# Optimization experiments

Measured on AMD Instinct MI355X. Metric: run time of the kernel, lower is better.

Reference implementation:

```python
import jax, jax.numpy as jnp
import numpy as np

L, K, H = 8192, 30, 128
SCALE = 30.0
LN_EPS = 1e-5


def _ln(x, g, b):
    mu = jnp.mean(x, axis=-1, keepdims=True)
    var = jnp.mean((x - mu) ** 2, axis=-1, keepdims=True)
    return (x - mu) * jax.lax.rsqrt(var + LN_EPS) * g + b


def _gelu(x):
    return jax.nn.gelu(x, approximate=False)  # torch.nn.GELU default (exact)


def setup_inputs() -> dict:
    key = jax.random.key(0)
    ks = jax.random.split(key, 16)

    def lin(k, din, dout):
        k1, k2 = jax.random.split(k)
        w = jax.random.normal(k1, (din, dout), jnp.float32) / np.sqrt(din).astype(np.float32)
        b = jax.random.normal(k2, (dout,), jnp.float32) * 0.01
        return w, b

    inp = {}
    inp['h_V'] = jax.random.normal(ks[0], (L, H), jnp.float32)
    inp['h_E'] = jax.random.normal(ks[1], (L, K, H), jnp.float32)
    inp['E_idx'] = jax.random.randint(ks[2], (L, K), 0, L, jnp.int32)
    inp['mask_V'] = jnp.ones((L,), jnp.float32)
    inp['mask_attend'] = jnp.ones((L, K), jnp.float32)

    D_in = 3 * H  # num_hidden + num_in = 128 + 256
    inp['W1'], inp['b1'] = lin(ks[3], D_in, H)
    inp['W2'], inp['b2'] = lin(ks[4], H, H)
    inp['W3'], inp['b3'] = lin(ks[5], H, H)
    inp['W11'], inp['b11'] = lin(ks[6], D_in, H)
    inp['W12'], inp['b12'] = lin(ks[7], H, H)
    inp['W13'], inp['b13'] = lin(ks[8], H, H)
    inp['Wi'], inp['bi'] = lin(ks[9], H, 4 * H)   # PositionWiseFeedForward.W_in
    inp['Wo'], inp['bo'] = lin(ks[10], 4 * H, H)  # PositionWiseFeedForward.W_out
    inp['g1'] = jnp.ones((H,), jnp.float32); inp['be1'] = jnp.zeros((H,), jnp.float32)
    inp['g2'] = jnp.ones((H,), jnp.float32); inp['be2'] = jnp.zeros((H,), jnp.float32)
    inp['g3'] = jnp.ones((H,), jnp.float32); inp['be3'] = jnp.zeros((H,), jnp.float32)
    return inp


def _forward(h_V, h_E, E_idx, mask_V, mask_attend,
             W1, b1, W2, b2, W3, b3, W11, b11, W12, b12, W13, b13,
             Wi, bi, Wo, bo, g1, be1, g2, be2, g3, be3):
    # --- node update: gather neighbors, concat, 3-layer MLP message, masked sum ---
    h_nb = h_V[E_idx]                                   # [L,K,H] gather_nodes
    h_EV = jnp.concatenate(
        [jnp.broadcast_to(h_V[:, None, :], (L, K, H)), h_E, h_nb], axis=-1)  # [L,K,3H]
    m = _gelu(h_EV @ W1 + b1)
    m = _gelu(m @ W2 + b2)
    m = m @ W3 + b3                                     # [L,K,H]
    m = mask_attend[..., None] * m
    dh = jnp.sum(m, axis=-2) / SCALE                    # [L,H]
    h_V = _ln(h_V + dh, g1, be1)
    # --- position-wise FFN ---
    dh = _gelu(h_V @ Wi + bi) @ Wo + bo
    h_V = _ln(h_V + dh, g2, be2)
    h_V = mask_V[:, None] * h_V
    # --- edge update ---
    h_nb = h_V[E_idx]
    h_EV = jnp.concatenate(
        [jnp.broadcast_to(h_V[:, None, :], (L, K, H)), h_E, h_nb], axis=-1)
    m = _gelu(h_EV @ W11 + b11)
    m = _gelu(m @ W12 + b12)
    m = m @ W13 + b13
    h_E = _ln(h_E + m, g3, be3)
    return h_V, h_E


def reference(h_V, h_E, E_idx, mask_V, mask_attend,
              W1, b1, W2, b2, W3, b3, W11, b11, W12, b12, W13, b13,
              Wi, bi, Wo, bo, g1, be1, g2, be2, g3, be3):
    return _forward(h_V, h_E, E_idx, mask_V, mask_attend,
                    W1, b1, W2, b2, W3, b3, W11, b11, W12, b12, W13, b13,
                    Wi, bi, Wo, bo, g1, be1, g2, be2, g3, be3)
```

## Files before the change

### kernel.cpp

```cpp
#include <hip/hip_runtime.h>
#include <math.h>

typedef unsigned short u16;
typedef __bf16 bf16x8 __attribute__((ext_vector_type(8)));
typedef float f32x4 __attribute__((ext_vector_type(4)));
typedef u16 u16x8 __attribute__((ext_vector_type(8)));

#define LTOT 8192
#define KNB  30
#define HDIM 128

__device__ __forceinline__ float bf2f(u16 u){
  unsigned x = ((unsigned)u) << 16;
  return __builtin_bit_cast(float, x);
}
__device__ __forceinline__ u16 f2bf(float f){
  __bf16 h = (__bf16)f;
  return __builtin_bit_cast(u16, h);
}
__device__ __forceinline__ float fast_exp2(float x){
#if __has_builtin(__builtin_amdgcn_exp2f)
  return __builtin_amdgcn_exp2f(x);
#else
  return exp2f(x);
#endif
}
__device__ __forceinline__ float gelu_f(float x){
  float x2 = x * x;
  float g  = x * (2.3022082f + 0.10294324f * x2);
  float e  = fast_exp2(g);
  float r  = __builtin_amdgcn_rcpf(e + 1.f);
  return x * (1.f - r);
}
__device__ __forceinline__ void pack8(u16* dst, const float* s){
  float4 a = *(const float4*)s, b = *(const float4*)(s + 4);
  u16x8 p;
  p[0]=f2bf(a.x); p[1]=f2bf(a.y); p[2]=f2bf(a.z); p[3]=f2bf(a.w);
  p[4]=f2bf(b.x); p[5]=f2bf(b.y); p[6]=f2bf(b.z); p[7]=f2bf(b.w);
  *(u16x8*)dst = p;
}

struct TEnt { const float* src; u16* dst; int K; int N; int nb; };
struct TTab { TEnt e[12]; };

__global__ __launch_bounds__(256) void transpose_kernel(TTab t){
  int b = (int)blockIdx.x;
  for (int i = 0; i < 12; ++i){
    int nb = t.e[i].nb;
    if (b < nb){
      int N = t.e[i].N, Kd = t.e[i].K;
      int idx = b * 256 + (int)threadIdx.x;
      if (idx < Kd * N){
        int k = idx / N;
        int n = idx - k * N;
        t.e[i].dst[n * Kd + k] = f2bf(t.e[i].src[(long)k * N + n]);
      }
      return;
    }
    b -= nb;
  }
}

template<bool XF32>
__global__ __launch_bounds__(256) void pre_gemm_kernel(
  const void* __restrict__ X,
  const u16* __restrict__ WTa, const float* __restrict__ ba, u16* __restrict__ outa,
  const u16* __restrict__ WTc, u16* __restrict__ outc)
{
  __shared__ __align__(16) char smem[8704];
  u16* Xs = (u16*)smem;
  const int tid = threadIdx.x;
  const int wave = tid >> 6, lane = tid & 63, q = lane >> 4, s = lane & 15;
  const int row0 = (int)blockIdx.x * 32;

  for (int i = tid; i < 32 * 16; i += 256){
    int r = i >> 4, cb = i & 15;
    if (XF32) pack8(&Xs[r * 136 + cb * 8], &((const float*)X)[(long)(row0 + r) * HDIM + cb * 8]);
    else *(u16x8*)&Xs[r * 136 + cb * 8] = *(const u16x8*)&((const u16*)X)[(long)(row0 + r) * HDIM + cb * 8];
  }
  __syncthreads();
  for (int w = 0; w < 2; ++w){
    const u16* W = w ? WTc : WTa;
    u16* out = w ? outc : outa;
    f32x4 acc[2][2];
#pragma unroll
    for (int mt = 0; mt < 2; ++mt)
#pragma unroll
      for (int nt = 0; nt < 2; ++nt){ f32x4 z = {0.f,0.f,0.f,0.f}; acc[mt][nt] = z; }
    for (int kt = 0; kt < 4; ++kt){
      bf16x8 b0 = *(const bf16x8*)&W[(wave * 32 + s) * 128 + kt * 32 + q * 8];
      bf16x8 b1 = *(const bf16x8*)&W[(wave * 32 + 16 + s) * 128 + kt * 32 + q * 8];
#pragma unroll
      for (int mt = 0; mt < 2; ++mt){
        bf16x8 af = *(const bf16x8*)&Xs[(mt * 16 + s) * 136 + kt * 32 + q * 8];
        acc[mt][0] = __builtin_amdgcn_mfma_f32_16x16x32_bf16(af, b0, acc[mt][0], 0, 0, 0);
        acc[mt][1] = __builtin_amdgcn_mfma_f32_16x16x32_bf16(af, b1, acc[mt][1], 0, 0, 0);
      }
    }
#pragma unroll
    for (int nt = 0; nt < 2; ++nt){
      int col = wave * 32 + nt * 16 + s;
      float bv = w ? 0.f : ba[col];
#pragma unroll
      for (int mt = 0; mt < 2; ++mt)
#pragma unroll
        for (int r = 0; r < 4; ++r){
          int row = row0 + mt * 16 + q * 4 + r;
          out[(long)row * HDIM + col] = f2bf(acc[mt][nt][r] + bv);
        }
    }
  }
}

template<bool EDGE>
__global__ __launch_bounds__(256, 4) void msg_kernel(
  const float* __restrict__ hVin,
  const float* __restrict__ hE,
  const int* __restrict__ Eidx,
  const float* __restrict__ maskA,
  const u16* __restrict__ vsum,
  const u16* __restrict__ vcg,
  const u16* __restrict__ WTb, const u16* __restrict__ WT2, const u16* __restrict__ WT3,
  const float* __restrict__ b2, const float* __restrict__ b3,
  const float* __restrict__ gam, const float* __restrict__ bet,
  float* __restrict__ out_f32,
  u16* __restrict__ out_b16,
  float* __restrict__ outE)
{
  __shared__ __align__(16) char smem[36352];
  u16*   As   = (u16*)smem;
  float* ovl  = (float*)smem;
  u16*   Vs   = (u16*)(smem + 17408);
  float* vbuf = (float*)(smem + 34816);
  float* mbuf = (float*)(smem + 35840);
  int*   nbr  = (int*)(smem + 36096);

  const int tid = threadIdx.x;
  const int wave = tid >> 6, lane = tid & 63, q = lane >> 4, s = lane & 15;
  const int node0 = (int)blockIdx.x * 2;

  for (int i = tid; i < 64 * 16; i += 256){
    int r = i >> 4, cb = i & 15, nd = r >> 5, k = r & 31;
    if (k < KNB)
      pack8(&As[r * 136 + cb * 8], &hE[(((long)(node0 + nd) * KNB) + k) * HDIM + cb * 8]);
    else { u16x8 z = {0,0,0,0,0,0,0,0}; *(u16x8*)&As[r * 136 + cb * 8] = z; }
  }
  if (tid < 64){
    int nd = tid >> 5, k = tid & 31;
    int e = (node0 + nd) * KNB + k;
    bool v = (k < KNB);
    nbr[tid] = v ? Eidx[e] : 0;
    if (!EDGE) mbuf[tid] = v ? maskA[e] : 0.f;
  }
  vbuf[tid] = bf2f(vsum[(long)(node0 + (tid >> 7)) * HDIM + (tid & 127)]);

  __syncthreads();

  for (int i = tid; i < 64 * 16; i += 256){
    int r = i >> 4, cb = i & 15;
    *(u16x8*)&Vs[r * 136 + cb * 8] = *(const u16x8*)&vcg[(long)nbr[r] * HDIM + cb * 8];
  }

  f32x4 acc[4][2];
  for (int layer = 0; layer < 3; ++layer){
    const u16* W = (layer == 0) ? WTb : ((layer == 1) ? WT2 : WT3);
    if (layer) __syncthreads();
#pragma unroll
    for (int mt = 0; mt < 4; ++mt){ f32x4 z = {0.f,0.f,0.f,0.f}; acc[mt][0] = z; acc[mt][1] = z; }
    for (int kt = 0; kt < 4; ++kt){
      bf16x8 b0 = *(const bf16x8*)&W[(wave * 32 + s) * 128 + kt * 32 + q * 8];
      bf16x8 b1 = *(const bf16x8*)&W[(wave * 32 + 16 + s) * 128 + kt * 32 + q * 8];
#pragma unroll
      for (int mt = 0; mt < 4; ++mt){
        bf16x8 af = *(const bf16x8*)&As[(mt * 16 + s) * 136 + kt * 32 + q * 8];
        acc[mt][0] = __builtin_amdgcn_mfma_f32_16x16x32_bf16(af, b0, acc[mt][0], 0, 0, 0);
        acc[mt][1] = __builtin_amdgcn_mfma_f32_16x16x32_bf16(af, b1, acc[mt][1], 0, 0, 0);
      }
    }
    if (layer < 2){
      __syncthreads();
#pragma unroll
      for (int nt = 0; nt < 2; ++nt){
        int col = wave * 32 + nt * 16 + s;
        float bv = (layer == 1) ? b2[col] : 0.f;
        float vb0 = 0.f, vb1 = 0.f;
        if (layer == 0){ vb0 = vbuf[col]; vb1 = vbuf[128 + col]; }
#pragma unroll
        for (int mt = 0; mt < 4; ++mt)
#pragma unroll
          for (int r = 0; r < 4; ++r){
            int row = mt * 16 + q * 4 + r;
            float v = acc[mt][nt][r] + bv;
            if (layer == 0)
              v += (mt < 2 ? vb0 : vb1) + bf2f(Vs[row * 136 + col]);
            As[row * 136 + col] = f2bf(gelu_f(v));
          }
      }
    }
  }
  __syncthreads();

  if (!EDGE){
    float* dh = ovl;
#pragma unroll
    for (int nt = 0; nt < 2; ++nt){
      int col = wave * 32 + nt * 16 + s;
      float b3v = b3[col];
#pragma unroll
      for (int ni = 0; ni < 2; ++ni){
        float ss = 0.f;
#pragma unroll
        for (int mh = 0; mh < 2; ++mh){
          int mt = ni * 2 + mh;
#pragma unroll
          for (int r = 0; r < 4; ++r){
            int row = mt * 16 + q * 4 + r;
            ss += (acc[mt][nt][r] + b3v) * mbuf[row];
          }
        }
        ss += __shfl_xor(ss, 16);
        ss += __shfl_xor(ss, 32);
        if (q == 0) dh[ni * 128 + col] = ss * (1.f / 30.f);
      }
    }
    __syncthreads();
    if (wave < 2){
      int node = node0 + wave;
      float x0 = hVin[(long)node * HDIM + lane]      + dh[wave * 128 + lane];
      float x1 = hVin[(long)node * HDIM + 64 + lane] + dh[wave * 128 + 64 + lane];
      float sm = x0 + x1, s2 = x0 * x0 + x1 * x1;
#pragma unroll
      for (int o = 32; o; o >>= 1){ sm += __shfl_xor(sm, o); s2 += __shfl_xor(s2, o); }
      float mu = sm * (1.f / 128.f);
      float var = fmaxf(s2 * (1.f / 128.f) - mu * mu, 0.f);
      float rs = rsqrtf(var + 1e-5f);
      float y0 = (x0 - mu) * rs * gam[lane]      + bet[lane];
      float y1 = (x1 - mu) * rs * gam[64 + lane] + bet[64 + lane];
      out_f32[(long)node * HDIM + lane]      = y0;
      out_f32[(long)node * HDIM + 64 + lane] = y1;
      out_b16[(long)node * HDIM + lane]      = f2bf(y0);
      out_b16[(long)node * HDIM + 64 + lane] = f2bf(y1);
    }
  } else {
    float* part  = ovl;
    float* part2 = ovl + 256;
    float* muv   = ovl + 512;
    float* rsv   = ovl + 576;
#pragma unroll
    for (int nt = 0; nt < 2; ++nt){
      int col = wave * 32 + nt * 16 + s;
      float b3v = b3[col];
#pragma unroll
      for (int mt = 0; mt < 4; ++mt)
#pragma unroll
        for (int r = 0; r < 4; ++r){
          int row = mt * 16 + q * 4 + r, nd = row >> 5, k = row & 31;
          float z = acc[mt][nt][r] + b3v;
          if (k < KNB) z += hE[(((long)(node0 + nd) * KNB) + k) * HDIM + col];
          acc[mt][nt][r] = z;
        }
    }
#pragma unroll
    for (int mt = 0; mt < 4; ++mt)
#pragma unroll
      for (int r = 0; r < 4; ++r){
        int row = mt * 16 + q * 4 + r;
        float ps = acc[mt][0][r] + acc[mt][1][r];
        float pq = acc[mt][0][r] * acc[mt][0][r] + acc[mt][1][r] * acc[mt][1][r];
#pragma unroll
        for (int o = 1; o < 16; o <<= 1){ ps += __shfl_xor(ps, o); pq += __shfl_xor(pq, o); }
        if (s == 0){ part[row * 4 + wave] = ps; part2[row * 4 + wave] = pq; }
      }
    __syncthreads();
    if (tid < 64){
      float sm = part[tid*4] + part[tid*4+1] + part[tid*4+2] + part[tid*4+3];
      float sq = part2[tid*4] + part2[tid*4+1] + part2[tid*4+2] + part2[tid*4+3];
      float mu = sm * (1.f / 128.f);
      float var = fmaxf(sq * (1.f / 128.f) - mu * mu, 0.f);
      muv[tid] = mu;
      rsv[tid] = rsqrtf(var + 1e-5f);
    }
    __syncthreads();
#pragma unroll
    for (int nt = 0; nt < 2; ++nt){
      int col = wave * 32 + nt * 16 + s;
      float gv = gam[col], bv = bet[col];
#pragma unroll
      for (int mt = 0; mt < 4; ++mt)
#pragma unroll
        for (int r = 0; r < 4; ++r){
          int row = mt * 16 + q * 4 + r, nd = row >> 5, k = row & 31;
          if (k < KNB){
            float y = (acc[mt][nt][r] - muv[row]) * rsv[row] * gv + bv;
            outE[(((long)(node0 + nd) * KNB) + k) * HDIM + col] = y;
          }
        }
    }
  }
}

__global__ __launch_bounds__(256) void ffn_kernel(
  const u16* __restrict__ xb, const float* __restrict__ xf,
  const u16* __restrict__ WiT,
  const u16* __restrict__ WoT,
  const float* __restrict__ bi, const float* __restrict__ bo,
  const float* __restrict__ g2, const float* __restrict__ be2,
  const float* __restrict__ maskV,
  float* __restrict__ outV, u16* __restrict__ hv2)
{
  __shared__ __align__(16) char smem[18816];
  u16*   Xs = (u16*)smem;
  u16*   Ts = (u16*)(smem + 8704);
  float* part  = (float*)(smem + 17408);
  float* part2 = part + 128;
  float* muv   = part + 256;
  float* rsv   = part + 288;
  const int tid = threadIdx.x;
  const int wave = tid >> 6, lane = tid & 63, q = lane >> 4, s = lane & 15;
  const int row0 = (int)blockIdx.x * 32;

  for (int i = tid; i < 32 * 16; i += 256){
    int r = i >> 4, cb = i & 15;
    *(u16x8*)&Xs[r * 136 + cb * 8] = *(const u16x8*)&xb[(long)(row0 + r) * HDIM + cb * 8];
  }
  f32x4 yac[2][2];
#pragma unroll
  for (int mt = 0; mt < 2; ++mt)
#pragma unroll
    for (int nt = 0; nt < 2; ++nt){ f32x4 z = {0.f,0.f,0.f,0.f}; yac[mt][nt] = z; }

  for (int j = 0; j < 4; ++j){
    __syncthreads();
    f32x4 tac[2][2];
#pragma unroll
    for (int mt = 0; mt < 2; ++mt)
#pragma unroll
      for (int nt = 0; nt < 2; ++nt){ f32x4 z = {0.f,0.f,0.f,0.f}; tac[mt][nt] = z; }
    for (int kt = 0; kt < 4; ++kt){
      bf16x8 b0 = *(const bf16x8*)&WiT[((long)(j * 128 + wave * 32 + s)) * 128 + kt * 32 + q * 8];
      bf16x8 b1 = *(const bf16x8*)&WiT[((long)(j * 128 + wave * 32 + 16 + s)) * 128 + kt * 32 + q * 8];
#pragma unroll
      for (int mt = 0; mt < 2; ++mt){
        bf16x8 af = *(const bf16x8*)&Xs[(mt * 16 + s) * 136 + kt * 32 + q * 8];
        tac[mt][0] = __builtin_amdgcn_mfma_f32_16x16x32_bf16(af, b0, tac[mt][0], 0, 0, 0);
        tac[mt][1] = __builtin_amdgcn_mfma_f32_16x16x32_bf16(af, b1, tac[mt][1], 0, 0, 0);
      }
    }
#pragma unroll
    for (int nt = 0; nt < 2; ++nt){
      int col = wave * 32 + nt * 16 + s;
      float bv = bi[j * 128 + col];
#pragma unroll
      for (int mt = 0; mt < 2; ++mt)
#pragma unroll
        for (int r = 0; r < 4; ++r){
          int row = mt * 16 + q * 4 + r;
          Ts[row * 136 + col] = f2bf(gelu_f(tac[mt][nt][r] + bv));
        }
    }
    __syncthreads();
    for (int kt = 0; kt < 4; ++kt){
      bf16x8 b0 = *(const bf16x8*)&WoT[((long)(wave * 32 + s)) * 512 + j * 128 + kt * 32 + q * 8];
      bf16x8 b1 = *(const bf16x8*)&WoT[((long)(wave * 32 + 16 + s)) * 512 + j * 128 + kt * 32 + q * 8];
#pragma unroll
      for (int mt = 0; mt < 2; ++mt){
        bf16x8 af = *(const bf16x8*)&Ts[(mt * 16 + s) * 136 + kt * 32 + q * 8];
        yac[mt][0] = __builtin_amdgcn_mfma_f32_16x16x32_bf16(af, b0, yac[mt][0], 0, 0, 0);
        yac[mt][1] = __builtin_amdgcn_mfma_f32_16x16x32_bf16(af, b1, yac[mt][1], 0, 0, 0);
      }
    }
  }
#pragma unroll
  for (int nt = 0; nt < 2; ++nt){
    int col = wave * 32 + nt * 16 + s;
    float bv = bo[col];
#pragma unroll
    for (int mt = 0; mt < 2; ++mt)
#pragma unroll
      for (int r = 0; r < 4; ++r){
        int row = mt * 16 + q * 4 + r;
        yac[mt][nt][r] += bv + xf[(long)(row0 + row) * HDIM + col];
      }
  }
#pragma unroll
  for (int mt = 0; mt < 2; ++mt)
#pragma unroll
    for (int r = 0; r < 4; ++r){
      int row = mt * 16 + q * 4 + r;
      float ps = yac[mt][0][r] + yac[mt][1][r];
      float pq = yac[mt][0][r] * yac[mt][0][r] + yac[mt][1][r] * yac[mt][1][r];
#pragma unroll
      for (int o = 1; o < 16; o <<= 1){ ps += __shfl_xor(ps, o); pq += __shfl_xor(pq, o); }
      if (s == 0){ part[row * 4 + wave] = ps; part2[row * 4 + wave] = pq; }
    }
  __syncthreads();
  if (tid < 32){
    float sm = part[tid*4] + part[tid*4+1] + part[tid*4+2] + part[tid*4+3];
    float sq = part2[tid*4] + part2[tid*4+1] + part2[tid*4+2] + part2[tid*4+3];
    float mu = sm * (1.f / 128.f);
    float var = fmaxf(sq * (1.f / 128.f) - mu * mu, 0.f);
    muv[tid] = mu;
    rsv[tid] = rsqrtf(var + 1e-5f);
  }
  __syncthreads();
#pragma unroll
  for (int nt = 0; nt < 2; ++nt){
    int col = wave * 32 + nt * 16 + s;
    float gv = g2[col], bv = be2[col];
#pragma unroll
    for (int mt = 0; mt < 2; ++mt)
#pragma unroll
      for (int r = 0; r < 4; ++r){
        int row = mt * 16 + q * 4 + r;
        float y = (yac[mt][nt][r] - muv[row]) * rsv[row] * gv + bv;
        y *= maskV[row0 + row];
        outV[(long)(row0 + row) * HDIM + col] = y;
        hv2[(long)(row0 + row) * HDIM + col] = f2bf(y);
      }
  }
}

extern "C" void kernel_launch(void* const* d_in, const int* in_sizes, int n_in,
                              void* d_out, int out_size, void* d_ws, size_t ws_size,
                              hipStream_t stream) {
  const float* hV    = (const float*)d_in[0];
  const float* hE    = (const float*)d_in[1];
  const int*   Eidx  = (const int*)d_in[2];
  const float* maskV = (const float*)d_in[3];
  const float* maskA = (const float*)d_in[4];
  const float* W1  = (const float*)d_in[5];  const float* b1  = (const float*)d_in[6];
  const float* W2  = (const float*)d_in[7];  const float* b2  = (const float*)d_in[8];
  const float* W3  = (const float*)d_in[9];  const float* b3  = (const float*)d_in[10];
  const float* W11 = (const float*)d_in[11]; const float* b11 = (const float*)d_in[12];
  const float* W12 = (const float*)d_in[13]; const float* b12 = (const float*)d_in[14];
  const float* W13 = (const float*)d_in[15]; const float* b13 = (const float*)d_in[16];
  const float* Wi  = (const float*)d_in[17]; const float* bi  = (const float*)d_in[18];
  const float* Wo  = (const float*)d_in[19]; const float* bo  = (const float*)d_in[20];
  const float* g1  = (const float*)d_in[21]; const float* be1 = (const float*)d_in[22];
  const float* g2  = (const float*)d_in[23]; const float* be2 = (const float*)d_in[24];
  const float* g3  = (const float*)d_in[25]; const float* be3 = (const float*)d_in[26];

  char* ws = (char*)d_ws;
  u16* wt = (u16*)ws;
  u16* wtW1a  = wt;
  u16* wtW1b  = wt + 16384;
  u16* wtW1c  = wt + 32768;
  u16* wtW2   = wt + 49152;
  u16* wtW3   = wt + 65536;
  u16* wtW11a = wt + 81920;
  u16* wtW11b = wt + 98304;
  u16* wtW11c = wt + 114688;
  u16* wtW12  = wt + 131072;
  u16* wtW13  = wt + 147456;
  u16* wtWi   = wt + 163840;
  u16* wtWo   = wt + 229376;
  size_t off = 589824;
  u16* vsum1   = (u16*)(ws + off); off += 2097152;
  u16* vc      = (u16*)(ws + off); off += 2097152;
  u16* vsum11  = (u16*)(ws + off); off += 2097152;
  u16* vc2     = (u16*)(ws + off); off += 2097152;
  float* hv1_f32 = (float*)(ws + off); off += 4194304;
  u16*   hv1_b16 = (u16*)(ws + off);   off += 2097152;
  u16*   hv2_b16 = (u16*)(ws + off);   off += 2097152;

  float* outV = (float*)d_out;
  float* outE = (float*)d_out + (long)LTOT * HDIM;

  TTab tt;
  tt.e[0]  = { W1,          wtW1a,  128, 128, 64 };
  tt.e[1]  = { W1 + 16384,  wtW1b,  128, 128, 64 };
  tt.e[2]  = { W1 + 32768,  wtW1c,  128, 128, 64 };
  tt.e[3]  = { W2,          wtW2,   128, 128, 64 };
  tt.e[4]  = { W3,          wtW3,   128, 128, 64 };
  tt.e[5]  = { W11,         wtW11a, 128, 128, 64 };
  tt.e[6]  = { W11 + 16384, wtW11b, 128, 128, 64 };
  tt.e[7]  = { W11 + 32768, wtW11c, 128, 128, 64 };
  tt.e[8]  = { W12,         wtW12,  128, 128, 64 };
  tt.e[9]  = { W13,         wtW13,  128, 128, 64 };
  tt.e[10] = { Wi,          wtWi,   128, 512, 256 };
  tt.e[11] = { Wo,          wtWo,   512, 128, 256 };
  transpose_kernel<<<dim3(1152), dim3(256), 0, stream>>>(tt);

  pre_gemm_kernel<true><<<dim3(256), dim3(256), 0, stream>>>(
      hV, wtW1a, b1, vsum1, wtW1c, vc);
  msg_kernel<false><<<dim3(4096), dim3(256), 0, stream>>>(
      hV, hE, Eidx, maskA, vsum1, vc, wtW1b, wtW2, wtW3, b2, b3, g1, be1,
      hv1_f32, hv1_b16, nullptr);
  ffn_kernel<<<dim3(256), dim3(256), 0, stream>>>(
      hv1_b16, hv1_f32, wtWi, wtWo, bi, bo, g2, be2, maskV, outV, hv2_b16);
  pre_gemm_kernel<false><<<dim3(256), dim3(256), 0, stream>>>(
      hv2_b16, wtW11a, b11, vsum11, wtW11c, vc2);
  msg_kernel<true><<<dim3(4096), dim3(256), 0, stream>>>(
      hV, hE, Eidx, maskA, vsum11, vc2, wtW11b, wtW12, wtW13, b12, b13, g3, be3,
      hv1_f32, hv1_b16, outE);
}
```

Before: 442.5 us.

## Fuse second pre-GEMM into FFN kernel and halve row tiles for more blocks

The edge-update pre-GEMM (W11a/W11c projections) now runs inside the FFN kernel on the LayerNorm output held in shared memory. This removes one kernel launch and the round trip of the bf16 hv2 buffer through global memory. The FFN tile shrinks from 32 to 16 rows, giving 512 blocks instead of 256 for better occupancy on the many CUs, at the cost of reloading FFN weights twice as often. The first pre_gemm is split so each block computes one of the two projections, doubling its grid.

```diff
diff --git a/kernel.cpp b/kernel.cpp
--- a/kernel.cpp
+++ b/kernel.cpp
@@ -61,9 +61,8 @@
   }
 }
 
-template<bool XF32>
 __global__ __launch_bounds__(256) void pre_gemm_kernel(
-  const void* __restrict__ X,
+  const float* __restrict__ X,
   const u16* __restrict__ WTa, const float* __restrict__ ba, u16* __restrict__ outa,
   const u16* __restrict__ WTc, u16* __restrict__ outc)
 {
@@ -71,44 +70,42 @@
   u16* Xs = (u16*)smem;
   const int tid = threadIdx.x;
   const int wave = tid >> 6, lane = tid & 63, q = lane >> 4, s = lane & 15;
-  const int row0 = (int)blockIdx.x * 32;
+  const int w = (int)blockIdx.x & 1;
+  const int row0 = ((int)blockIdx.x >> 1) * 32;
 
   for (int i = tid; i < 32 * 16; i += 256){
     int r = i >> 4, cb = i & 15;
-    if (XF32) pack8(&Xs[r * 136 + cb * 8], &((const float*)X)[(long)(row0 + r) * HDIM + cb * 8]);
-    else *(u16x8*)&Xs[r * 136 + cb * 8] = *(const u16x8*)&((const u16*)X)[(long)(row0 + r) * HDIM + cb * 8];
+    pack8(&Xs[r * 136 + cb * 8], &X[(long)(row0 + r) * HDIM + cb * 8]);
   }
   __syncthreads();
-  for (int w = 0; w < 2; ++w){
-    const u16* W = w ? WTc : WTa;
-    u16* out = w ? outc : outa;
-    f32x4 acc[2][2];
+  const u16* W = w ? WTc : WTa;
+  u16* out = w ? outc : outa;
+  f32x4 acc[2][2];
+#pragma unroll
+  for (int mt = 0; mt < 2; ++mt)
+#pragma unroll
+    for (int nt = 0; nt < 2; ++nt){ f32x4 z = {0.f,0.f,0.f,0.f}; acc[mt][nt] = z; }
+  for (int kt = 0; kt < 4; ++kt){
+    bf16x8 b0 = *(const bf16x8*)&W[(wave * 32 + s) * 128 + kt * 32 + q * 8];
+    bf16x8 b1 = *(const bf16x8*)&W[(wave * 32 + 16 + s) * 128 + kt * 32 + q * 8];
+#pragma unroll
+    for (int mt = 0; mt < 2; ++mt){
+      bf16x8 af = *(const bf16x8*)&Xs[(mt * 16 + s) * 136 + kt * 32 + q * 8];
+      acc[mt][0] = __builtin_amdgcn_mfma_f32_16x16x32_bf16(af, b0, acc[mt][0], 0, 0, 0);
+      acc[mt][1] = __builtin_amdgcn_mfma_f32_16x16x32_bf16(af, b1, acc[mt][1], 0, 0, 0);
+    }
+  }
+#pragma unroll
+  for (int nt = 0; nt < 2; ++nt){
+    int col = wave * 32 + nt * 16 + s;
+    float bv = w ? 0.f : ba[col];
 #pragma unroll
     for (int mt = 0; mt < 2; ++mt)
 #pragma unroll
-      for (int nt = 0; nt < 2; ++nt){ f32x4 z = {0.f,0.f,0.f,0.f}; acc[mt][nt] = z; }
-    for (int kt = 0; kt < 4; ++kt){
-      bf16x8 b0 = *(const bf16x8*)&W[(wave * 32 + s) * 128 + kt * 32 + q * 8];
-      bf16x8 b1 = *(const bf16x8*)&W[(wave * 32 + 16 + s) * 128 + kt * 32 + q * 8];
-#pragma unroll
-      for (int mt = 0; mt < 2; ++mt){
-        bf16x8 af = *(const bf16x8*)&Xs[(mt * 16 + s) * 136 + kt * 32 + q * 8];
-        acc[mt][0] = __builtin_amdgcn_mfma_f32_16x16x32_bf16(af, b0, acc[mt][0], 0, 0, 0);
-        acc[mt][1] = __builtin_amdgcn_mfma_f32_16x16x32_bf16(af, b1, acc[mt][1], 0, 0, 0);
-      }
-    }
-#pragma unroll
-    for (int nt = 0; nt < 2; ++nt){
-      int col = wave * 32 + nt * 16 + s;
-      float bv = w ? 0.f : ba[col];
-#pragma unroll
-      for (int mt = 0; mt < 2; ++mt)
-#pragma unroll
-        for (int r = 0; r < 4; ++r){
-          int row = row0 + mt * 16 + q * 4 + r;
-          out[(long)row * HDIM + col] = f2bf(acc[mt][nt][r] + bv);
-        }
-    }
+      for (int r = 0; r < 4; ++r){
+        int row = row0 + mt * 16 + q * 4 + r;
+        out[(long)row * HDIM + col] = f2bf(acc[mt][nt][r] + bv);
+      }
   }
 }
 
@@ -306,68 +303,64 @@
   const float* __restrict__ bi, const float* __restrict__ bo,
   const float* __restrict__ g2, const float* __restrict__ be2,
   const float* __restrict__ maskV,
-  float* __restrict__ outV, u16* __restrict__ hv2)
+  const u16* __restrict__ W11aT, const float* __restrict__ b11,
+  const u16* __restrict__ W11cT,
+  float* __restrict__ outV, u16* __restrict__ vsum11, u16* __restrict__ vc2)
 {
-  __shared__ __align__(16) char smem[18816];
+  __shared__ __align__(16) char smem[13696];
   u16*   Xs = (u16*)smem;
-  u16*   Ts = (u16*)(smem + 8704);
-  float* part  = (float*)(smem + 17408);
-  float* part2 = part + 128;
-  float* muv   = part + 256;
-  float* rsv   = part + 288;
+  u16*   Ts = (u16*)(smem + 4352);
+  u16*   Ys = (u16*)(smem + 8704);
+  float* part  = (float*)(smem + 13056);
+  float* part2 = part + 64;
+  float* muv   = part + 128;
+  float* rsv   = part + 144;
   const int tid = threadIdx.x;
   const int wave = tid >> 6, lane = tid & 63, q = lane >> 4, s = lane & 15;
-  const int row0 = (int)blockIdx.x * 32;
-
-  for (int i = tid; i < 32 * 16; i += 256){
-    int r = i >> 4, cb = i & 15;
+  const int row0 = (int)blockIdx.x * 16;
+
+  float resid[2][4];
+#pragma unroll
+  for (int nt = 0; nt < 2; ++nt)
+#pragma unroll
+    for (int r = 0; r < 4; ++r)
+      resid[nt][r] = xf[(long)(row0 + q * 4 + r) * HDIM + wave * 32 + nt * 16 + s];
+
+  {
+    int r = tid >> 4, cb = tid & 15;
     *(u16x8*)&Xs[r * 136 + cb * 8] = *(const u16x8*)&xb[(long)(row0 + r) * HDIM + cb * 8];
   }
-  f32x4 yac[2][2];
-#pragma unroll
-  for (int mt = 0; mt < 2; ++mt)
-#pragma unroll
-    for (int nt = 0; nt < 2; ++nt){ f32x4 z = {0.f,0.f,0.f,0.f}; yac[mt][nt] = z; }
+  f32x4 yac[2];
+  { f32x4 z = {0.f,0.f,0.f,0.f}; yac[0] = z; yac[1] = z; }
 
   for (int j = 0; j < 4; ++j){
     __syncthreads();
-    f32x4 tac[2][2];
-#pragma unroll
-    for (int mt = 0; mt < 2; ++mt)
-#pragma unroll
-      for (int nt = 0; nt < 2; ++nt){ f32x4 z = {0.f,0.f,0.f,0.f}; tac[mt][nt] = z; }
+    f32x4 tac[2];
+    { f32x4 z = {0.f,0.f,0.f,0.f}; tac[0] = z; tac[1] = z; }
     for (int kt = 0; kt < 4; ++kt){
       bf16x8 b0 = *(const bf16x8*)&WiT[((long)(j * 128 + wave * 32 + s)) * 128 + kt * 32 + q * 8];
       bf16x8 b1 = *(const bf16x8*)&WiT[((long)(j * 128 + wave * 32 + 16 + s)) * 128 + kt * 32 + q * 8];
-#pragma unroll
-      for (int mt = 0; mt < 2; ++mt){
-        bf16x8 af = *(const bf16x8*)&Xs[(mt * 16 + s) * 136 + kt * 32 + q * 8];
-        tac[mt][0] = __builtin_amdgcn_mfma_f32_16x16x32_bf16(af, b0, tac[mt][0], 0, 0, 0);
-        tac[mt][1] = __builtin_amdgcn_mfma_f32_16x16x32_bf16(af, b1, tac[mt][1], 0, 0, 0);
-      }
+      bf16x8 af = *(const bf16x8*)&Xs[s * 136 + kt * 32 + q * 8];
+      tac[0] = __builtin_amdgcn_mfma_f32_16x16x32_bf16(af, b0, tac[0], 0, 0, 0);
+      tac[1] = __builtin_amdgcn_mfma_f32_16x16x32_bf16(af, b1, tac[1], 0, 0, 0);
     }
 #pragma unroll
     for (int nt = 0; nt < 2; ++nt){
       int col = wave * 32 + nt * 16 + s;
       float bv = bi[j * 128 + col];
 #pragma unroll
-      for (int mt = 0; mt < 2; ++mt)
-#pragma unroll
-        for (int r = 0; r < 4; ++r){
-          int row = mt * 16 + q * 4 + r;
-          Ts[row * 136 + col] = f2bf(gelu_f(tac[mt][nt][r] + bv));
-        }
+      for (int r = 0; r < 4; ++r){
+        int row = q * 4 + r;
+        Ts[row * 136 + col] = f2bf(gelu_f(tac[nt][r] + bv));
+      }
     }
     __syncthreads();
     for (int kt = 0; kt < 4; ++kt){
       bf16x8 b0 = *(const bf16x8*)&WoT[((long)(wave * 32 + s)) * 512 + j * 128 + kt * 32 + q * 8];
       bf16x8 b1 = *(const bf16x8*)&WoT[((long)(wave * 32 + 16 + s)) * 512 + j * 128 + kt * 32 + q * 8];
-#pragma unroll
-      for (int mt = 0; mt < 2; ++mt){
-        bf16x8 af = *(const bf16x8*)&Ts[(mt * 16 + s) * 136 + kt * 32 + q * 8];
-        yac[mt][0] = __builtin_amdgcn_mfma_f32_16x16x32_bf16(af, b0, yac[mt][0], 0, 0, 0);
-        yac[mt][1] = __builtin_amdgcn_mfma_f32_16x16x32_bf16(af, b1, yac[mt][1], 0, 0, 0);
-      }
+      bf16x8 af = *(const bf16x8*)&Ts[s * 136 + kt * 32 + q * 8];
+      yac[0] = __builtin_amdgcn_mfma_f32_16x16x32_bf16(af, b0, yac[0], 0, 0, 0);
+      yac[1] = __builtin_amdgcn_mfma_f32_16x16x32_bf16(af, b1, yac[1], 0, 0, 0);
     }
   }
 #pragma unroll
@@ -375,26 +368,20 @@
     int col = wave * 32 + nt * 16 + s;
     float bv = bo[col];
 #pragma unroll
-    for (int mt = 0; mt < 2; ++mt)
-#pragma unroll
-      for (int r = 0; r < 4; ++r){
-        int row = mt * 16 + q * 4 + r;
-        yac[mt][nt][r] += bv + xf[(long)(row0 + row) * HDIM + col];
-      }
-  }
-#pragma unroll
-  for (int mt = 0; mt < 2; ++mt)
-#pragma unroll
-    for (int r = 0; r < 4; ++r){
-      int row = mt * 16 + q * 4 + r;
-      float ps = yac[mt][0][r] + yac[mt][1][r];
-      float pq = yac[mt][0][r] * yac[mt][0][r] + yac[mt][1][r] * yac[mt][1][r];
-#pragma unroll
-      for (int o = 1; o < 16; o <<= 1){ ps += __shfl_xor(ps, o); pq += __shfl_xor(pq, o); }
-      if (s == 0){ part[row * 4 + wave] = ps; part2[row * 4 + wave] = pq; }
-    }
+    for (int r = 0; r < 4; ++r)
+      yac[nt][r] += bv + resid[nt][r];
+  }
+#pragma unroll
+  for (int r = 0; r < 4; ++r){
+    int row = q * 4 + r;
+    float ps = yac[0][r] + yac[1][r];
+    float pq = yac[0][r] * yac[0][r] + yac[1][r] * yac[1][r];
+#pragma unroll
+    for (int o = 1; o < 16; o <<= 1){ ps += __shfl_xor(ps, o); pq += __shfl_xor(pq, o); }
+    if (s == 0){ part[row * 4 + wave] = ps; part2[row * 4 + wave] = pq; }
+  }
   __syncthreads();
-  if (tid < 32){
+  if (tid < 16){
     float sm = part[tid*4] + part[tid*4+1] + part[tid*4+2] + part[tid*4+3];
     float sq = part2[tid*4] + part2[tid*4+1] + part2[tid*4+2] + part2[tid*4+3];
     float mu = sm * (1.f / 128.f);
@@ -408,15 +395,37 @@
     int col = wave * 32 + nt * 16 + s;
     float gv = g2[col], bv = be2[col];
 #pragma unroll
-    for (int mt = 0; mt < 2; ++mt)
+    for (int r = 0; r < 4; ++r){
+      int row = q * 4 + r;
+      float y = (yac[nt][r] - muv[row]) * rsv[row] * gv + bv;
+      y *= maskV[row0 + row];
+      outV[(long)(row0 + row) * HDIM + col] = y;
+      Ys[row * 136 + col] = f2bf(y);
+    }
+  }
+  __syncthreads();
+  for (int w = 0; w < 2; ++w){
+    const u16* W = w ? W11cT : W11aT;
+    u16* out = w ? vc2 : vsum11;
+    f32x4 acc[2];
+    { f32x4 z = {0.f,0.f,0.f,0.f}; acc[0] = z; acc[1] = z; }
+    for (int kt = 0; kt < 4; ++kt){
+      bf16x8 b0 = *(const bf16x8*)&W[(wave * 32 + s) * 128 + kt * 32 + q * 8];
+      bf16x8 b1 = *(const bf16x8*)&W[(wave * 32 + 16 + s) * 128 + kt * 32 + q * 8];
+      bf16x8 af = *(const bf16x8*)&Ys[s * 136 + kt * 32 + q * 8];
+      acc[0] = __builtin_amdgcn_mfma_f32_16x16x32_bf16(af, b0, acc[0], 0, 0, 0);
+      acc[1] = __builtin_amdgcn_mfma_f32_16x16x32_bf16(af, b1, acc[1], 0, 0, 0);
+    }
+#pragma unroll
+    for (int nt = 0; nt < 2; ++nt){
+      int col = wave * 32 + nt * 16 + s;
+      float bv = w ? 0.f : b11[col];
 #pragma unroll
       for (int r = 0; r < 4; ++r){
-        int row = mt * 16 + q * 4 + r;
-        float y = (yac[mt][nt][r] - muv[row]) * rsv[row] * gv + bv;
-        y *= maskV[row0 + row];
-        outV[(long)(row0 + row) * HDIM + col] = y;
-        hv2[(long)(row0 + row) * HDIM + col] = f2bf(y);
-      }
+        int row = row0 + q * 4 + r;
+        out[(long)row * HDIM + col] = f2bf(acc[nt][r] + bv);
+      }
+    }
   }
 }
 
@@ -461,7 +470,6 @@
   u16* vc2     = (u16*)(ws + off); off += 2097152;
   float* hv1_f32 = (float*)(ws + off); off += 4194304;
   u16*   hv1_b16 = (u16*)(ws + off);   off += 2097152;
-  u16*   hv2_b16 = (u16*)(ws + off);   off += 2097152;
 
   float* outV = (float*)d_out;
   float* outE = (float*)d_out + (long)LTOT * HDIM;
@@ -481,15 +489,14 @@
   tt.e[11] = { Wo,          wtWo,   512, 128, 256 };
   transpose_kernel<<<dim3(1152), dim3(256), 0, stream>>>(tt);
 
-  pre_gemm_kernel<true><<<dim3(256), dim3(256), 0, stream>>>(
+  pre_gemm_kernel<<<dim3(512), dim3(256), 0, stream>>>(
       hV, wtW1a, b1, vsum1, wtW1c, vc);
   msg_kernel<false><<<dim3(4096), dim3(256), 0, stream>>>(
       hV, hE, Eidx, maskA, vsum1, vc, wtW1b, wtW2, wtW3, b2, b3, g1, be1,
       hv1_f32, hv1_b16, nullptr);
-  ffn_kernel<<<dim3(256), dim3(256), 0, stream>>>(
-      hv1_b16, hv1_f32, wtWi, wtWo, bi, bo, g2, be2, maskV, outV, hv2_b16);
-  pre_gemm_kernel<false><<<dim3(256), dim3(256), 0, stream>>>(
-      hv2_b16, wtW11a, b11, vsum11, wtW11c, vc2);
+  ffn_kernel<<<dim3(512), dim3(256), 0, stream>>>(
+      hv1_b16, hv1_f32, wtWi, wtWo, bi, bo, g2, be2, maskV,
+      wtW11a, b11, wtW11c, outV, vsum11, vc2);
   msg_kernel<true><<<dim3(4096), dim3(256), 0, stream>>>(
       hV, hE, Eidx, maskA, vsum11, vc2, wtW11b, wtW12, wtW13, b12, b13, g3, be3,
       hv1_f32, hv1_b16, outE);
```

Result: no change. 446.4 us (+0.9%).
